# Performance work log

Hardware: AMD Instinct MI355X
Metric: run time of the kernel (lower is better)

The kernel has to match this reference:

```python
import jax, jax.numpy as jnp
import numpy as np

NUM_PTM_TYPES = 26
NUM_PER_TYPE = 128
TEMPERATURE = 0.07


def setup_inputs() -> dict:
    key = jax.random.key(0)
    k1, k2, k3 = jax.random.split(key, 3)
    N, D = 8192, 256
    x = jax.random.normal(k1, (N, D), dtype=jnp.float32)
    Q = jax.random.randint(k2, (N,), 0, NUM_PTM_TYPES)
    E = jax.random.normal(k3, (NUM_PTM_TYPES * NUM_PER_TYPE, D), dtype=jnp.float32)
    E = E / jnp.linalg.norm(E, axis=1, keepdims=True)  # matches _initialize_embeddings
    return {"x": x, "Q": Q, "E": E, "tau": 1}


def _quantize_grouped(x, Q, E, tau):
    # Vectorized form of the per-PTM-type loop: every type owns an equal-size
    # sub-codebook of NUM_PER_TYPE rows, so gather each token's sub-codebook.
    D = x.shape[-1]
    cb = E.reshape(NUM_PTM_TYPES, NUM_PER_TYPE, D)[Q]          # [N, K, D]
    dot = jnp.einsum('nd,nkd->nk', x, cb) / tau                # [N, K]
    sim = jax.nn.softmax(dot, axis=-1)
    z_q = jnp.einsum('nk,nkd->nd', sim, cb)                    # [N, D]
    idx = jnp.argmax(sim, axis=-1) + Q * NUM_PER_TYPE          # global code index
    return z_q, idx


def _uniform_loss(E):
    K = E.shape[0]
    En = E / jnp.linalg.norm(E, axis=1, keepdims=True)
    sim = En @ En.T                                            # [K, K]
    labels = jnp.arange(K) // NUM_PER_TYPE
    labels_eq = labels[None, :] == labels[:, None]
    eye = jnp.eye(K, dtype=bool)
    sim = jnp.where(eye, -jnp.inf, sim)
    sim_exp = jnp.exp(sim / TEMPERATURE)                       # diagonal -> 0
    sum_exp = jnp.sum(sim_exp, axis=1)
    pos_sum_exp = jnp.sum(sim_exp * labels_eq.astype(sim_exp.dtype), axis=1)
    return -jnp.mean(jnp.log(pos_sum_exp / sum_exp))


def reference(x, Q, E, tau):
    tau = jnp.float32(tau)
    quantized, encoding_indices = _quantize_grouped(x, Q, E, tau)
    loss = jnp.float32(0.0)
    uniform_loss = _uniform_loss(E)
    return quantized, loss, uniform_loss, encoding_indices
```

## Files before the change

kernel.cpp:

```cpp
#include <hip/hip_runtime.h>
#include <hip/hip_bf16.h>

#define NUM_TYPES 26
#define NPT 128
#define DIMS 256
#define K_TOTAL 3328
#define N_TOK 8192
#define INV_TEMP (1.0f/0.07f)
#define TM 16
#define MAX_TILES 32
#define NHIST 32

typedef unsigned short ushort_t;
typedef short bf16x8 __attribute__((ext_vector_type(8)));
typedef float f32x4 __attribute__((ext_vector_type(4)));

__device__ __forceinline__ float wave_reduce_sum(float v){
#pragma unroll
  for (int off = 32; off; off >>= 1) v += __shfl_xor(v, off);
  return v;
}

__device__ __forceinline__ unsigned short f2bf(float f){
  __hip_bfloat16 h = __float2bfloat16(f);
  return __builtin_bit_cast(unsigned short, h);
}

#define GLOAD_LDS16(g, s) \
  __builtin_amdgcn_global_load_lds((__attribute__((address_space(1))) void*)(g), \
                                   (__attribute__((address_space(3))) void*)(s), 16, 0, 0)

#define VMWAIT(N) do{ asm volatile("s_waitcnt vmcnt(" #N ")" ::: "memory"); \
                      __builtin_amdgcn_sched_barrier(0); }while(0)

__global__ __launch_bounds__(256) void prepk(const float* __restrict__ E,
                                             const int* __restrict__ Q,
                                             ushort_t* __restrict__ Enb,
                                             float* __restrict__ EA,
                                             ushort_t* __restrict__ EC,
                                             int* __restrict__ bh){
  const int t = threadIdx.x;
  const int b = blockIdx.x;
  if (b < 832){
    const int w = t >> 6, l = t & 63;
    const int row = b * 4 + w;
    float4 v = reinterpret_cast<const float4*>(E + (size_t)row * DIMS)[l];
    float ss = v.x*v.x + v.y*v.y + v.z*v.z + v.w*v.w;
    ss = wave_reduce_sum(ss);
    const float inv = 1.0f / sqrtf(ss);
    ushort4 o;
    o.x = f2bf(v.x * inv); o.y = f2bf(v.y * inv);
    o.z = f2bf(v.z * inv); o.w = f2bf(v.w * inv);
    reinterpret_cast<ushort4*>(Enb + (size_t)row * DIMS)[l] = o;
    return;
  }
  if (b < 936){
    const int id = b - 832;
    const int tp = id >> 2, ck = id & 3;
    __shared__ float T[32][260];
    const int row = t >> 3, sub = t & 7;
    const float* src = E + (size_t)(tp*NPT + ck*32 + row) * DIMS;
#pragma unroll
    for (int i = 0; i < 8; ++i){
      const int c4 = sub + 8*i;
      *(f32x4*)(&T[row][c4*4]) = *(const f32x4*)(src + c4*4);
    }
    __syncthreads();
    ushort_t* dst = EC + (size_t)(tp*4 + ck) * 8192;
#pragma unroll
    for (int i = 0; i < 4; ++i){
      const int si = t + i*256;
      const int sec = si >> 8, d = (si >> 2) & 63, s = si & 3;
      const int cb8 = (s ^ ((d >> 1) & 3)) * 8;
      union { bf16x8 v8; ushort_t u[8]; } pk;
#pragma unroll
      for (int j = 0; j < 8; ++j)
        pk.u[j] = f2bf(T[cb8 + j][sec*64 + d]);
      *(bf16x8*)(dst + (size_t)si*8) = pk.v8;
    }
    return;
  }
  if (b < 1144){
    const int id = b - 936;
    const int tp = id >> 3, kt = id & 7;
    float* dst = EA + (size_t)(tp*8 + kt) * 4096;
    const float* src = E + (size_t)tp * NPT * DIMS;
#pragma unroll
    for (int i = 0; i < 16; ++i){
      const int e = i*256 + t;
      const int sec = e >> 10, code = (e >> 3) & 127, hp = (e >> 2) & 1, j = e & 3;
      const int dim = sec*64 + kt*8 + (hp ^ ((code >> 2) & 1))*4 + j;
      dst[e] = src[(size_t)code*DIMS + dim];
    }
    return;
  }
  {
    __shared__ int h[NUM_TYPES];
    if (t < NUM_TYPES) h[t] = 0;
    __syncthreads();
    const int c = b - 1144;
    atomicAdd(&h[Q[c*256 + t]], 1);
    __syncthreads();
    if (t < NUM_TYPES) bh[c*NUM_TYPES + t] = h[t];
  }
}

__global__ __launch_bounds__(256) void gramk(const ushort_t* __restrict__ Enb,
                                             const int* __restrict__ Q,
                                             const int* __restrict__ bh,
                                             int* __restrict__ counts,
                                             int* __restrict__ offsets,
                                             int* __restrict__ perm,
                                             float* __restrict__ part){
  const int bi = blockIdx.y, bj = blockIdx.x;
  const int t = threadIdx.x;
  if (bi > bj){
    const int lid = bi*(bi-1)/2 + bj;
    if (lid >= NHIST) return;
    __shared__ int sh_tot[NUM_TYPES], sh_off[NUM_TYPES], sh_cur[NUM_TYPES];
    if (t < NUM_TYPES){
      int s = 0;
      for (int h = 0; h < NHIST; ++h) s += bh[h*NUM_TYPES + t];
      sh_tot[t] = s;
    }
    __syncthreads();
    if (t == 0){
      int s = 0;
      for (int g = 0; g < NUM_TYPES; ++g){ sh_off[g] = s; s += sh_tot[g]; }
    }
    __syncthreads();
    if (t < NUM_TYPES){
      int run = sh_off[t];
      for (int h = 0; h < lid; ++h) run += bh[h*NUM_TYPES + t];
      sh_cur[t] = run;
      if (lid == 0){ counts[t] = sh_tot[t]; offsets[t] = sh_off[t]; }
    }
    __syncthreads();
    const int i = lid*256 + t;
    const int q = Q[i];
    const int pos = atomicAdd(&sh_cur[q], 1);
    perm[pos] = i;
    return;
  }
  __shared__ ushort_t As[128*64];
  __shared__ ushort_t Bs[128*64];
  __shared__ float rs[128][2];
  __shared__ float cs[128][2];
  const int w = t >> 6, l = t & 63;
  const int wr = w >> 1, wc = w & 1;
  const int lrow = l & 15;
  const int lk = (l >> 4) * 8;
  const int hi = l >> 4;

  f32x4 acc[4][4];
#pragma unroll
  for (int m = 0; m < 4; ++m)
#pragma unroll
    for (int n = 0; n < 4; ++n) acc[m][n] = (f32x4){0.f, 0.f, 0.f, 0.f};

  for (int kt = 0; kt < 4; ++kt){
    if (kt) __syncthreads();
#pragma unroll
    for (int p = 0; p < 4; ++p){
      const int cbase = p*256 + w*64;
      const int c = cbase + l;
      const int row = c >> 3;
      const int kcol = (c & 7) * 8;
      const ushort_t* gA = Enb + (size_t)(bi*128 + row) * DIMS + kt*64 + kcol;
      const ushort_t* gB = Enb + (size_t)(bj*128 + row) * DIMS + kt*64 + kcol;
      GLOAD_LDS16(gA, As + (size_t)cbase*8);
      GLOAD_LDS16(gB, Bs + (size_t)cbase*8);
    }
    __syncthreads();
#pragma unroll
    for (int kk = 0; kk < 2; ++kk){
      bf16x8 a[4], b[4];
#pragma unroll
      for (int m = 0; m < 4; ++m)
        a[m] = *reinterpret_cast<const bf16x8*>(&As[(wr*64 + m*16 + lrow)*64 + kk*32 + lk]);
#pragma unroll
      for (int n = 0; n < 4; ++n)
        b[n] = *reinterpret_cast<const bf16x8*>(&Bs[(wc*64 + n*16 + lrow)*64 + kk*32 + lk]);
#pragma unroll
      for (int m = 0; m < 4; ++m)
#pragma unroll
        for (int n = 0; n < 4; ++n)
          acc[m][n] = __builtin_amdgcn_mfma_f32_16x16x32_bf16(a[m], b[n], acc[m][n], 0, 0, 0);
    }
  }

#pragma unroll
  for (int m = 0; m < 4; ++m)
#pragma unroll
    for (int n = 0; n < 4; ++n)
#pragma unroll
      for (int j = 0; j < 4; ++j){
        const int grow = bi*128 + wr*64 + m*16 + hi*4 + j;
        const int gcol = bj*128 + wc*64 + n*16 + lrow;
        const float g = acc[m][n][j];
        acc[m][n][j] = (grow == gcol) ? 0.f : __expf(g * INV_TEMP);
      }

#pragma unroll
  for (int m = 0; m < 4; ++m)
#pragma unroll
    for (int j = 0; j < 4; ++j){
      float s = 0.f;
#pragma unroll
      for (int n = 0; n < 4; ++n) s += acc[m][n][j];
#pragma unroll
      for (int off = 1; off < 16; off <<= 1) s += __shfl_xor(s, off);
      if (lrow == 0) rs[wr*64 + m*16 + hi*4 + j][wc] = s;
    }
  if (bi != bj){
#pragma unroll
    for (int n = 0; n < 4; ++n){
      float c = 0.f;
#pragma unroll
      for (int m = 0; m < 4; ++m)
#pragma unroll
        for (int j = 0; j < 4; ++j) c += acc[m][n][j];
      c += __shfl_xor(c, 16); c += __shfl_xor(c, 32);
      if (hi == 0) cs[wc*64 + n*16 + lrow][wr] = c;
    }
  }
  __syncthreads();
  if (t < 128){
    part[(size_t)bj*K_TOTAL + bi*128 + t] = rs[t][0] + rs[t][1];
    if (bi != bj)
      part[(size_t)bi*K_TOTAL + bj*128 + t] = cs[t][0] + cs[t][1];
  }
}

__device__ __forceinline__ void stageA3(const float* EA, char* dst, int tp, int kt,
                                        int w, int l){
  const char* src = (const char*)(EA + (size_t)(tp*8 + kt) * 4096) + w*4096;
  char* d = dst + w*4096;
#pragma unroll
  for (int i = 0; i < 4; ++i)
    GLOAD_LDS16(src + i*1024 + l*16, d + i*1024);
}

__device__ __forceinline__ void stageC3(const ushort_t* EC, char* dst, int tp, int ck,
                                        int w, int l){
  const char* src = (const char*)(EC + (size_t)(tp*4 + ck) * 8192) + w*4096;
  char* d = dst + w*4096;
#pragma unroll
  for (int i = 0; i < 4; ++i)
    GLOAD_LDS16(src + i*1024 + l*16, d + i*1024);
}

__global__ __launch_bounds__(256, 2) void quantg(const float* __restrict__ x,
                                                 const float* __restrict__ EA,
                                                 const ushort_t* __restrict__ EC,
                                                 const float* __restrict__ part,
                                                 const int* __restrict__ counts,
                                                 const int* __restrict__ offsets,
                                                 const int* __restrict__ perm,
                                                 const int* __restrict__ taup,
                                                 float* __restrict__ outZ,
                                                 float* __restrict__ outMisc,
                                                 float* __restrict__ outIdx){
  const int t = threadIdx.x;
  const int tp = blockIdx.x, rb = blockIdx.y;
  __shared__ __align__(16) char arena[65664];

  if (tp == NUM_TYPES){
    if (rb) return;
    float acc = 0.f;
    for (int i = t; i < K_TOTAL; i += 256){
      float s = 0.f;
#pragma unroll
      for (int bb = 0; bb < NUM_TYPES; ++bb) s += part[(size_t)bb*K_TOTAL + i];
      acc += logf(s) - logf(part[(size_t)(i >> 7)*K_TOTAL + i]);
    }
    acc = wave_reduce_sum(acc);
    float* red = (float*)arena;
    if ((t & 63) == 0) red[t >> 6] = acc;
    __syncthreads();
    if (t == 0){ outMisc[0] = 0.f; outMisc[1] = (red[0]+red[1]+red[2]+red[3]) / (float)K_TOTAL; }
    return;
  }

  const int cnt = counts[tp];
  if (rb * TM >= cnt) return;
  const int nt = min(TM, cnt - rb * TM);
  const int off = offsets[tp] + rb * TM;

  char* XA = arena;
  char* BA = arena + 16384;
  char* PB = arena + 16384;
  char* SB = arena;
  char* BC = arena + 16384;
  int* tids = (int*)(arena + 65600);

  const int w = t >> 6, l = t & 63;
  const int tx = l & 15, ty = l >> 4;

  const int ti = *taup;
  const float tau = (ti > 0 && ti < (1 << 23)) ? (float)ti : __int_as_float(ti);
  const float inv_tau = 1.0f / tau;

  if (t < TM) tids[t] = (t < nt) ? perm[off + t] : 0;

#pragma unroll
  for (int r = 0; r < 4; ++r){
    const int row = r*4 + w;
    const int tid = (row < nt) ? perm[off + row] : 0;
    const int sc = (l & 56) | ((l & 7) ^ (row & 7));
    GLOAD_LDS16(x + (size_t)tid*DIMS + sc*4, XA + row*1024);
  }
  stageA3(EA, BA,         tp, 0, w, l);
  stageA3(EA, BA + 16384, tp, 1, w, l);
  __syncthreads();

  float acc[4][8];
#pragma unroll
  for (int rr = 0; rr < 4; ++rr)
#pragma unroll
    for (int cc = 0; cc < 8; ++cc) acc[rr][cc] = 0.f;

#pragma unroll
  for (int kt = 0; kt < 8; ++kt){
    if (kt < 6) stageA3(EA, BA + ((kt+2)%3)*16384, tp, kt+2, w, l);
    if (kt >= 2){
      if (kt < 6)      { VMWAIT(8); }
      else if (kt == 6){ VMWAIT(4); }
      else             { VMWAIT(0); }
    }
    const char* bbuf = BA + (kt%3)*16384 + w*4096;
#pragma unroll
    for (int q = 0; q < 2; ++q){
      f32x4 a[4], b[8];
#pragma unroll
      for (int rr = 0; rr < 4; ++rr){
        const int row = ty*4 + rr;
        const int c = (w*16 + kt*2 + q) ^ (row & 7);
        a[rr] = *(const f32x4*)(XA + row*1024 + c*16);
      }
#pragma unroll
      for (int cc = 0; cc < 8; ++cc){
        const int code = tx + 16*cc;
        const int slot = q ^ ((code >> 2) & 1);
        b[cc] = *(const f32x4*)(bbuf + code*32 + slot*16);
      }
#pragma unroll
      for (int rr = 0; rr < 4; ++rr)
#pragma unroll
        for (int cc = 0; cc < 8; ++cc)
#pragma unroll
          for (int e = 0; e < 4; ++e)
            acc[rr][cc] = fmaf(a[rr][e], b[cc][e], acc[rr][cc]);
    }
  }
  __syncthreads();

#pragma unroll
  for (int rr = 0; rr < 4; ++rr)
#pragma unroll
    for (int cc = 0; cc < 8; ++cc)
      *(float*)(PB + w*8448 + (ty*4+rr)*528 + (tx + 16*cc)*4) = acc[rr][cc];
  __syncthreads();

  {
    const int r = t >> 4, s = t & 15;
    f32x4 v0 = (f32x4){0,0,0,0}, v1 = (f32x4){0,0,0,0};
#pragma unroll
    for (int ww = 0; ww < 4; ++ww){
      v0 += *(const f32x4*)(PB + ww*8448 + r*528 + s*32);
      v1 += *(const f32x4*)(PB + ww*8448 + r*528 + s*32 + 16);
    }
    float v[8];
#pragma unroll
    for (int e = 0; e < 4; ++e){ v[e] = v0[e]*inv_tau; v[4+e] = v1[e]*inv_tau; }
    float m = v[0]; int mi = s*8;
#pragma unroll
    for (int j = 1; j < 8; ++j) if (v[j] > m){ m = v[j]; mi = s*8 + j; }
#pragma unroll
    for (int o = 1; o < 16; o <<= 1){
      const float om = __shfl_xor(m, o);
      const int   oi = __shfl_xor(mi, o);
      if (om > m || (om == m && oi < mi)){ m = om; mi = oi; }
    }
    float e8[8]; float sum = 0.f;
#pragma unroll
    for (int j = 0; j < 8; ++j){ e8[j] = __expf(v[j] - m); sum += e8[j]; }
#pragma unroll
    for (int o = 1; o < 16; o <<= 1) sum += __shfl_xor(sum, o);
    const float inv = 1.0f / sum;
    union { bf16x8 v8; ushort_t u[8]; } pk;
#pragma unroll
    for (int j = 0; j < 8; ++j) pk.u[j] = f2bf(e8[j] * inv);
    *(bf16x8*)(SB + r*272 + s*16) = pk.v8;
    if (s == 0 && r < nt)
      outIdx[tids[r]] = (float)(mi + tp * NPT);
  }
  __syncthreads();

  stageC3(EC, BC,         tp, 0, w, l);
  stageC3(EC, BC + 16384, tp, 1, w, l);
  f32x4 zacc[4];
#pragma unroll
  for (int n = 0; n < 4; ++n) zacc[n] = (f32x4){0,0,0,0};
#pragma unroll
  for (int ck = 0; ck < 4; ++ck){
    if (ck < 2) stageC3(EC, BC + ((ck+2)%3)*16384, tp, ck+2, w, l);
    if (ck < 2)      { VMWAIT(8); }
    else if (ck == 2){ VMWAIT(4); }
    else             { VMWAIT(0); }
    const bf16x8 af = *(const bf16x8*)(SB + tx*272 + ck*64 + ty*16);
    const char* bbuf = BC + (ck%3)*16384 + w*4096;
#pragma unroll
    for (int n = 0; n < 4; ++n){
      const int d = n*16 + tx;
      const int slot = ty ^ ((d >> 1) & 3);
      const bf16x8 bf = *(const bf16x8*)(bbuf + d*64 + slot*16);
      zacc[n] = __builtin_amdgcn_mfma_f32_16x16x32_bf16(af, bf, zacc[n], 0, 0, 0);
    }
  }
#pragma unroll
  for (int n = 0; n < 4; ++n)
#pragma unroll
    for (int j = 0; j < 4; ++j){
      const int row = ty*4 + j;
      if (row < nt)
        outZ[(size_t)tids[row]*DIMS + w*64 + n*16 + tx] = zacc[n][j];
    }
}

extern "C" void kernel_launch(void* const* d_in, const int* in_sizes, int n_in,
                              void* d_out, int out_size, void* d_ws, size_t ws_size,
                              hipStream_t stream){
  const float* x  = (const float*)d_in[0];
  const int*   Q  = (const int*)d_in[1];
  const float* E  = (const float*)d_in[2];
  const int* taup = (const int*)d_in[3];

  float* outZ    = (float*)d_out;
  float* outMisc = outZ + (size_t)N_TOK * DIMS;
  float* outIdx  = outMisc + 2;

  char* wsp = (char*)d_ws;
  ushort_t* Enb = (ushort_t*)wsp;
  float* part   = (float*)(wsp + 1703936);
  float* EA     = (float*)(wsp + 2050048);
  ushort_t* EC  = (ushort_t*)(wsp + 5457920);
  int* bh       = (int*)(wsp + 7161856);
  int* counts   = (int*)(wsp + 7165184);
  int* offsets  = (int*)(wsp + 7165312);
  int* perm     = (int*)(wsp + 7165440);

  prepk<<<1176, 256, 0, stream>>>(E, Q, Enb, EA, EC, bh);
  gramk<<<dim3(26, 26), 256, 0, stream>>>(Enb, Q, bh, counts, offsets, perm, part);
  quantg<<<dim3(NUM_TYPES + 1, MAX_TILES), 256, 0, stream>>>(x, EA, EC, part,
                                                             counts, offsets, perm,
                                                             taup, outZ, outMisc, outIdx);
}
```

Measured before the change: 50.07 us.

## Read codebook directly from global in dot phase and shrink LDS for occupancy

Codebook tiles for the fp32 dot-product phase are no longer staged into LDS through a triple-buffered pipeline. Each wave now loads its B operands straight from global memory, using a new layout that groups 8 dims contiguously per code, and the four waves are split into 2 D-halves by 2 code-halves. The partial-sum reduction shrinks from 4 to 2 buffers, and the z phase drops from triple to double buffering. Together these cut LDS from about 64KB to about 36KB so launch bounds can rise to 4 blocks per CU, at the cost of global or L2 latency on the B loads, which are no longer prefetched.

```diff
diff --git a/kernel.cpp b/kernel.cpp
--- a/kernel.cpp
+++ b/kernel.cpp
@@ -36,7 +36,7 @@
 __global__ __launch_bounds__(256) void prepk(const float* __restrict__ E,
                                              const int* __restrict__ Q,
                                              ushort_t* __restrict__ Enb,
-                                             float* __restrict__ EA,
+                                             float* __restrict__ EA2,
                                              ushort_t* __restrict__ EC,
                                              int* __restrict__ bh){
   const int t = threadIdx.x;
@@ -83,14 +83,13 @@
   if (b < 1144){
     const int id = b - 936;
     const int tp = id >> 3, kt = id & 7;
-    float* dst = EA + (size_t)(tp*8 + kt) * 4096;
+    float* dst = EA2 + (size_t)tp*32768 + kt*1024;
     const float* src = E + (size_t)tp * NPT * DIMS;
 #pragma unroll
     for (int i = 0; i < 16; ++i){
       const int e = i*256 + t;
-      const int sec = e >> 10, code = (e >> 3) & 127, hp = (e >> 2) & 1, j = e & 3;
-      const int dim = sec*64 + kt*8 + (hp ^ ((code >> 2) & 1))*4 + j;
-      dst[e] = src[(size_t)code*DIMS + dim];
+      const int sec = e >> 10, code = (e >> 3) & 127, j = e & 7;
+      dst[sec*8192 + code*8 + j] = src[(size_t)code*DIMS + sec*64 + kt*8 + j];
     }
     return;
   }
@@ -232,15 +231,6 @@
   }
 }
 
-__device__ __forceinline__ void stageA3(const float* EA, char* dst, int tp, int kt,
-                                        int w, int l){
-  const char* src = (const char*)(EA + (size_t)(tp*8 + kt) * 4096) + w*4096;
-  char* d = dst + w*4096;
-#pragma unroll
-  for (int i = 0; i < 4; ++i)
-    GLOAD_LDS16(src + i*1024 + l*16, d + i*1024);
-}
-
 __device__ __forceinline__ void stageC3(const ushort_t* EC, char* dst, int tp, int ck,
                                         int w, int l){
   const char* src = (const char*)(EC + (size_t)(tp*4 + ck) * 8192) + w*4096;
@@ -250,8 +240,8 @@
     GLOAD_LDS16(src + i*1024 + l*16, d + i*1024);
 }
 
-__global__ __launch_bounds__(256, 2) void quantg(const float* __restrict__ x,
-                                                 const float* __restrict__ EA,
+__global__ __launch_bounds__(256, 4) void quantg(const float* __restrict__ x,
+                                                 const float* __restrict__ EA2,
                                                  const ushort_t* __restrict__ EC,
                                                  const float* __restrict__ part,
                                                  const int* __restrict__ counts,
@@ -263,7 +253,7 @@
                                                  float* __restrict__ outIdx){
   const int t = threadIdx.x;
   const int tp = blockIdx.x, rb = blockIdx.y;
-  __shared__ __align__(16) char arena[65664];
+  __shared__ __align__(16) char arena[37120];
 
   if (tp == NUM_TYPES){
     if (rb) return;
@@ -288,85 +278,78 @@
   const int off = offsets[tp] + rb * TM;
 
   char* XA = arena;
-  char* BA = arena + 16384;
-  char* PB = arena + 16384;
-  char* SB = arena;
-  char* BC = arena + 16384;
-  int* tids = (int*)(arena + 65600);
+  char* PB = arena;
+  char* BC = arena;
+  char* SB = arena + 32768;
 
   const int w = t >> 6, l = t & 63;
+  const int h  = w >> 1;
+  const int cg = w & 1;
   const int tx = l & 15, ty = l >> 4;
 
   const int ti = *taup;
   const float tau = (ti > 0 && ti < (1 << 23)) ? (float)ti : __int_as_float(ti);
   const float inv_tau = 1.0f / tau;
 
-  if (t < TM) tids[t] = (t < nt) ? perm[off + t] : 0;
-
-#pragma unroll
-  for (int r = 0; r < 4; ++r){
-    const int row = r*4 + w;
-    const int tid = (row < nt) ? perm[off + row] : 0;
+#pragma unroll
+  for (int i = 0; i < 4; ++i){
+    const int row = w*4 + i;
+    const int tid = (row < nt) ? perm[off + row] : perm[off];
     const int sc = (l & 56) | ((l & 7) ^ (row & 7));
     GLOAD_LDS16(x + (size_t)tid*DIMS + sc*4, XA + row*1024);
   }
-  stageA3(EA, BA,         tp, 0, w, l);
-  stageA3(EA, BA + 16384, tp, 1, w, l);
   __syncthreads();
 
-  float acc[4][8];
+  float acc[4][4];
 #pragma unroll
   for (int rr = 0; rr < 4; ++rr)
 #pragma unroll
-    for (int cc = 0; cc < 8; ++cc) acc[rr][cc] = 0.f;
-
-#pragma unroll
-  for (int kt = 0; kt < 8; ++kt){
-    if (kt < 6) stageA3(EA, BA + ((kt+2)%3)*16384, tp, kt+2, w, l);
-    if (kt >= 2){
-      if (kt < 6)      { VMWAIT(8); }
-      else if (kt == 6){ VMWAIT(4); }
-      else             { VMWAIT(0); }
-    }
-    const char* bbuf = BA + (kt%3)*16384 + w*4096;
+    for (int cc = 0; cc < 4; ++cc) acc[rr][cc] = 0.f;
+
+  const float* ea = EA2 + (size_t)tp*32768 + h*16384;
+#pragma unroll
+  for (int kk = 0; kk < 16; ++kk){
+    f32x4 b0[4], b1[4];
+#pragma unroll
+    for (int cc = 0; cc < 4; ++cc){
+      const float* p = ea + (kk >> 3)*8192 + (kk & 7)*1024 + (size_t)(cg*64 + tx + 16*cc)*8;
+      b0[cc] = *(const f32x4*)(p);
+      b1[cc] = *(const f32x4*)(p + 4);
+    }
 #pragma unroll
     for (int q = 0; q < 2; ++q){
-      f32x4 a[4], b[8];
+      f32x4 a[4];
 #pragma unroll
       for (int rr = 0; rr < 4; ++rr){
-        const int row = ty*4 + rr;
-        const int c = (w*16 + kt*2 + q) ^ (row & 7);
+        const int row = rr*4 + ty;
+        const int c = (h*32 + kk*2 + q) ^ (row & 7);
         a[rr] = *(const f32x4*)(XA + row*1024 + c*16);
       }
 #pragma unroll
-      for (int cc = 0; cc < 8; ++cc){
-        const int code = tx + 16*cc;
-        const int slot = q ^ ((code >> 2) & 1);
-        b[cc] = *(const f32x4*)(bbuf + code*32 + slot*16);
-      }
-#pragma unroll
       for (int rr = 0; rr < 4; ++rr)
 #pragma unroll
-        for (int cc = 0; cc < 8; ++cc)
+        for (int cc = 0; cc < 4; ++cc)
 #pragma unroll
           for (int e = 0; e < 4; ++e)
-            acc[rr][cc] = fmaf(a[rr][e], b[cc][e], acc[rr][cc]);
+            acc[rr][cc] = fmaf(a[rr][e], (q ? b1 : b0)[cc][e], acc[rr][cc]);
     }
   }
   __syncthreads();
 
 #pragma unroll
-  for (int rr = 0; rr < 4; ++rr)
-#pragma unroll
-    for (int cc = 0; cc < 8; ++cc)
-      *(float*)(PB + w*8448 + (ty*4+rr)*528 + (tx + 16*cc)*4) = acc[rr][cc];
+  for (int rr = 0; rr < 4; ++rr){
+    const int row = rr*4 + ty;
+#pragma unroll
+    for (int cc = 0; cc < 4; ++cc)
+      *(float*)(PB + h*8448 + row*528 + (cg*64 + tx + 16*cc)*4) = acc[rr][cc];
+  }
   __syncthreads();
 
   {
     const int r = t >> 4, s = t & 15;
     f32x4 v0 = (f32x4){0,0,0,0}, v1 = (f32x4){0,0,0,0};
 #pragma unroll
-    for (int ww = 0; ww < 4; ++ww){
+    for (int ww = 0; ww < 2; ++ww){
       v0 += *(const f32x4*)(PB + ww*8448 + r*528 + s*32);
       v1 += *(const f32x4*)(PB + ww*8448 + r*528 + s*32 + 16);
     }
@@ -393,23 +376,21 @@
     for (int j = 0; j < 8; ++j) pk.u[j] = f2bf(e8[j] * inv);
     *(bf16x8*)(SB + r*272 + s*16) = pk.v8;
     if (s == 0 && r < nt)
-      outIdx[tids[r]] = (float)(mi + tp * NPT);
+      outIdx[perm[off + r]] = (float)(mi + tp * NPT);
   }
   __syncthreads();
 
-  stageC3(EC, BC,         tp, 0, w, l);
-  stageC3(EC, BC + 16384, tp, 1, w, l);
+  stageC3(EC, BC, tp, 0, w, l);
   f32x4 zacc[4];
 #pragma unroll
   for (int n = 0; n < 4; ++n) zacc[n] = (f32x4){0,0,0,0};
 #pragma unroll
   for (int ck = 0; ck < 4; ++ck){
-    if (ck < 2) stageC3(EC, BC + ((ck+2)%3)*16384, tp, ck+2, w, l);
-    if (ck < 2)      { VMWAIT(8); }
-    else if (ck == 2){ VMWAIT(4); }
+    if (ck < 3) stageC3(EC, BC + ((ck+1)&1)*16384, tp, ck+1, w, l);
+    if (ck < 3)      { VMWAIT(4); }
     else             { VMWAIT(0); }
     const bf16x8 af = *(const bf16x8*)(SB + tx*272 + ck*64 + ty*16);
-    const char* bbuf = BC + (ck%3)*16384 + w*4096;
+    const char* bbuf = BC + (ck&1)*16384 + w*4096;
 #pragma unroll
     for (int n = 0; n < 4; ++n){
       const int d = n*16 + tx;
@@ -424,7 +405,7 @@
     for (int j = 0; j < 4; ++j){
       const int row = ty*4 + j;
       if (row < nt)
-        outZ[(size_t)tids[row]*DIMS + w*64 + n*16 + tx] = zacc[n][j];
+        outZ[(size_t)perm[off + row]*DIMS + w*64 + n*16 + tx] = zacc[n][j];
     }
 }
 
@@ -443,16 +424,16 @@
   char* wsp = (char*)d_ws;
   ushort_t* Enb = (ushort_t*)wsp;
   float* part   = (float*)(wsp + 1703936);
-  float* EA     = (float*)(wsp + 2050048);
+  float* EA2    = (float*)(wsp + 2050048);
   ushort_t* EC  = (ushort_t*)(wsp + 5457920);
   int* bh       = (int*)(wsp + 7161856);
   int* counts   = (int*)(wsp + 7165184);
   int* offsets  = (int*)(wsp + 7165312);
   int* perm     = (int*)(wsp + 7165440);
 
-  prepk<<<1176, 256, 0, stream>>>(E, Q, Enb, EA, EC, bh);
+  prepk<<<1176, 256, 0, stream>>>(E, Q, Enb, EA2, EC, bh);
   gramk<<<dim3(26, 26), 256, 0, stream>>>(Enb, Q, bh, counts, offsets, perm, part);
-  quantg<<<dim3(NUM_TYPES + 1, MAX_TILES), 256, 0, stream>>>(x, EA, EC, part,
+  quantg<<<dim3(NUM_TYPES + 1, MAX_TILES), 256, 0, stream>>>(x, EA2, EC, part,
                                                              counts, offsets, perm,
                                                              taup, outZ, outMisc, outIdx);
 }
```

Result: faster. 45.87 us (-8.4%).
